# Optimization experiments

Hardware: AMD Instinct MI355X
Metric: run time of the kernel (lower is better)

The kernel has to match this reference:

```python
import jax, jax.numpy as jnp
import numpy as np

DIM = 1024
HEADS = 16
DIM_HEAD = 64
INNER = HEADS * DIM_HEAD  # 1024
SCALE = DIM_HEAD ** -0.5


def setup_inputs() -> dict:
    key = jax.random.key(0)
    ks = jax.random.split(key, 5)
    b, n = 4, 2048
    x = jax.random.normal(ks[0], (b, n, DIM), dtype=jnp.float32)
    # nn.Linear weights, stored as (in, out) for x @ W
    w_q = jax.random.normal(ks[1], (DIM, INNER), dtype=jnp.float32) / np.sqrt(DIM)
    w_kv = jax.random.normal(ks[2], (DIM, 2 * DIM_HEAD), dtype=jnp.float32) / np.sqrt(DIM)
    w_out = jax.random.normal(ks[3], (INNER, DIM), dtype=jnp.float32) / np.sqrt(INNER)
    b_out = jax.random.normal(ks[4], (DIM,), dtype=jnp.float32) * 0.01
    return {"x": x, "w_q": w_q, "w_kv": w_kv, "w_out": w_out, "b_out": b_out}


def reference(x, w_q, w_kv, w_out, b_out):
    b, n, _ = x.shape
    # Q: [b, h, n, d]; K/V: single shared head [b, n, d]
    q = (x @ w_q).reshape(b, n, HEADS, DIM_HEAD).transpose(0, 2, 1, 3)
    kv = x @ w_kv  # [b, n, 2d]
    k, v = kv[..., :DIM_HEAD], kv[..., DIM_HEAD:]
    # scores: broadcast shared K across heads
    dots = jnp.einsum('bhnd,bmd->bhnm', q, k) * SCALE  # [b,h,n,n]
    attn = jax.nn.softmax(dots, axis=-1)
    out = jnp.einsum('bhnm,bmd->bhnd', attn, v)  # shared V across heads
    out = out.transpose(0, 2, 1, 3).reshape(b, n, INNER)
    return out @ w_out + b_out
```

## Files before the change

### kernel.cpp

```cpp
#include <hip/hip_runtime.h>
#include <hip/hip_bf16.h>
#include <stdint.h>

#define SEQ    2048
#define NBATCH 4
#define NHEADS 16
#define DHEAD  64
#define MODELD 1024
#define QKVN   1152
#define MROWS  (NBATCH*SEQ)
#define SCALE_LOG2E 0.1803368801111244f

typedef __bf16 bf16x8 __attribute__((ext_vector_type(8)));
typedef float  f32x4  __attribute__((ext_vector_type(4)));

typedef __attribute__((address_space(1))) void* as1_void_p;
typedef __attribute__((address_space(3))) void* as3_void_p;

__device__ __forceinline__ void gld_lds16(const void* g, void* l) {
  __builtin_amdgcn_global_load_lds((as1_void_p)(g), (as3_void_p)(l), 16, 0, 0);
}

__device__ __forceinline__ ushort f2bf(float f) {
  union { float f; uint32_t i; } t; t.f = f;
  uint32_t r = (t.i + 0x7fffu + ((t.i >> 16) & 1u)) >> 16;
  return (ushort)r;
}
__device__ __forceinline__ uint32_t pack_bf16(float a, float b) {
  union { __hip_bfloat162 h2; uint32_t u; } cv;
  cv.h2 = __float22bfloat162_rn(make_float2(a, b));
  return cv.u;
}

__device__ __forceinline__ void do_transpose(const float* __restrict__ src,
                                             ushort* __restrict__ dst,
                                             int R, int C, float scale,
                                             int gx, int gy, int tid) {
  __shared__ float tile[32][33];
  const int tx = tid & 31, ty = tid >> 5;
  const int c0 = gx * 32, r0 = gy * 32;
#pragma unroll
  for (int j = 0; j < 4; j++)
    tile[ty*4 + j][tx] = src[(size_t)(r0 + ty*4 + j) * C + c0 + tx];
  __syncthreads();
#pragma unroll
  for (int j = 0; j < 4; j++)
    dst[(size_t)(c0 + ty*4 + j) * R + r0 + tx] = f2bf(tile[tx][ty*4 + j] * scale);
}

__global__ __launch_bounds__(256)
void prep(const float* __restrict__ x, const float* __restrict__ w_q,
          const float* __restrict__ w_kv, const float* __restrict__ w_out,
          ushort* __restrict__ xb, ushort* __restrict__ wqkvT,
          ushort* __restrict__ woutT) {
  const int bid = blockIdx.x, tid = threadIdx.x;
  if (bid < 8192) {
    const size_t i = ((size_t)bid * 256 + tid) * 4;
    const float4 v = *(const float4*)(x + i);
    ushort4 o;
    o.x = f2bf(v.x); o.y = f2bf(v.y); o.z = f2bf(v.z); o.w = f2bf(v.w);
    *(ushort4*)(xb + i) = o;
  } else if (bid < 9216) {
    const int t = bid - 8192;
    do_transpose(w_q, wqkvT, MODELD, MODELD, SCALE_LOG2E, t & 31, t >> 5, tid);
  } else if (bid < 9344) {
    const int t = bid - 9216;
    do_transpose(w_kv, wqkvT + (size_t)MODELD * MODELD, MODELD, 128, 1.0f,
                 t & 3, t >> 2, tid);
  } else {
    const int t = bid - 9344;
    do_transpose(w_out, woutT, MODELD, MODELD, 1.0f, t & 31, t >> 5, tid);
  }
}

template <bool OUT_F32>
__global__ __launch_bounds__(256)
void gemm_bt(const ushort* __restrict__ A, const ushort* __restrict__ Bt,
             void* __restrict__ Cp, const float* __restrict__ bias,
             ushort* __restrict__ VT,
             int K, int lda, int ldb, int ldc) {
  __shared__ __attribute__((aligned(16))) ushort As[128*64];
  __shared__ __attribute__((aligned(16))) ushort Bs[128*64];
  const int tid = threadIdx.x;
  const int w = tid >> 6, lane = tid & 63;
  const int quad = lane >> 4, m16 = lane & 15;

  const int nwg = gridDim.x * gridDim.y;
  const int orig = blockIdx.y * gridDim.x + blockIdx.x;
  const int qq = nwg >> 3, rr = nwg & 7;
  const int xcd = orig & 7, loc = orig >> 3;
  const int L = (xcd < rr ? xcd * (qq + 1) : rr * (qq + 1) + (xcd - rr) * qq) + loc;
  const int bm0 = (L / gridDim.x) * 128, bn0 = (L % gridDim.x) * 128;

  f32x4 acc[4][4] = {};

  const int sr = lane >> 3;
  const int sg = ((lane & 7) ^ (sr & 7)) * 8;
  const ushort* Ag = A  + (size_t)(bm0 + w*32 + sr) * lda + sg;
  const ushort* Bg = Bt + (size_t)(bn0 + w*32 + sr) * ldb + sg;
  ushort* AsW = As + (w*32)*64;
  ushort* BsW = Bs + (w*32)*64;
  const int wm = (w >> 1) * 64, wn = (w & 1) * 64;

  for (int kb = 0; kb < K; kb += 64) {
#pragma unroll
    for (int c = 0; c < 4; c++) {
      gld_lds16(Ag + (size_t)(c*8)*lda + kb, AsW + c*8*64);
      gld_lds16(Bg + (size_t)(c*8)*ldb + kb, BsW + c*8*64);
    }
    __syncthreads();
#pragma unroll
    for (int kk = 0; kk < 2; kk++) {
      bf16x8 af[4], bfr[4];
      const int rg = ((kk*4 + quad) ^ (m16 & 7)) * 8;
#pragma unroll
      for (int mi = 0; mi < 4; mi++)
        af[mi] = *(const bf16x8*)(As + (wm + mi*16 + m16)*64 + rg);
#pragma unroll
      for (int ni = 0; ni < 4; ni++)
        bfr[ni] = *(const bf16x8*)(Bs + (wn + ni*16 + m16)*64 + rg);
#pragma unroll
      for (int mi = 0; mi < 4; mi++)
#pragma unroll
        for (int ni = 0; ni < 4; ni++)
          acc[mi][ni] = __builtin_amdgcn_mfma_f32_16x16x32_bf16(
              af[mi], bfr[ni], acc[mi][ni], 0, 0, 0);
    }
    __syncthreads();
  }

  const bool blockHasV = (VT != nullptr) && (bn0 + 128 > 1088);
#pragma unroll
  for (int ni = 0; ni < 4; ni++) {
    const int col = bn0 + wn + ni*16 + m16;
    const float bv = bias ? bias[col] : 0.0f;
#pragma unroll
    for (int mi = 0; mi < 4; mi++) {
#pragma unroll
      for (int r = 0; r < 4; r++) {
        const int row = bm0 + wm + mi*16 + quad*4 + r;
        const float v = acc[mi][ni][r] + bv;
        if (OUT_F32) ((float*)Cp)[(size_t)row*ldc + col] = v;
        else         ((ushort*)Cp)[(size_t)row*ldc + col] = f2bf(v);
        if (blockHasV && col >= 1088) {
          const int d = col - 1088, bb = row >> 11, n = row & 2047;
          VT[((size_t)bb * DHEAD + d) * SEQ + n] = f2bf(v);
        }
      }
    }
  }
}

__global__ __launch_bounds__(256, 2)
void mqa_attn(const ushort* __restrict__ qkv, const ushort* __restrict__ vT,
              ushort* __restrict__ attn_out) {
  __shared__ __attribute__((aligned(16))) ushort Ks[64*72];
  __shared__ __attribute__((aligned(16))) ushort Vs[80*72];
  __shared__ __attribute__((aligned(16))) ushort pbuf[4][32*72];

  const int tid = threadIdx.x;
  const int w = tid >> 6, lane = tid & 63;
  const int quad = lane >> 4, m16 = lane & 15;
  const int h = blockIdx.y, b = blockIdx.z;
  const size_t rowbase = (size_t)b * SEQ;
  const int q0 = blockIdx.x * 128 + w * 32;
  const ushort* vTb = vT + (size_t)b * DHEAD * SEQ;
  ushort* pb = pbuf[w];

  for (int i = tid; i < 16*72; i += 256)
    Vs[64*72 + i] = (i < 72) ? (ushort)0x3F80 : (ushort)0;

  const int srow = tid >> 3, scol = (tid & 7) * 8;
  const ushort* kgbase = qkv + (rowbase + srow) * QKVN + 1024 + scol;
  const ushort* vgbase = vTb + (size_t)srow * SEQ + scol;

  bf16x8 qf[2][2];
#pragma unroll
  for (int qt = 0; qt < 2; qt++) {
    const ushort* qrow = qkv + (rowbase + q0 + qt*16 + m16) * QKVN + h * DHEAD;
    qf[qt][0] = *(const bf16x8*)(qrow + quad*8);
    qf[qt][1] = *(const bf16x8*)(qrow + 32 + quad*8);
  }

  f32x4 o[2][4] = {};
  f32x4 o4[2]   = {};

  uint4 kreg0 = *(const uint4*)(kgbase);
  uint4 kreg1 = *(const uint4*)(kgbase + (size_t)32 * QKVN);
  uint4 vreg0 = *(const uint4*)(vgbase);
  uint4 vreg1 = *(const uint4*)(vgbase + 32 * SEQ);

  for (int kv0 = 0; kv0 < SEQ; kv0 += 64) {
    __syncthreads();
    *(uint4*)(Ks + (srow     )*72 + scol) = kreg0;
    *(uint4*)(Ks + (srow + 32)*72 + scol) = kreg1;
    *(uint4*)(Vs + (srow     )*72 + scol) = vreg0;
    *(uint4*)(Vs + (srow + 32)*72 + scol) = vreg1;
    __syncthreads();

    const int kvn = (kv0 + 64) & (SEQ - 1);
    kreg0 = *(const uint4*)(kgbase + (size_t)(kvn     ) * QKVN);
    kreg1 = *(const uint4*)(kgbase + (size_t)(kvn + 32) * QKVN);
    vreg0 = *(const uint4*)(vgbase + kvn);
    vreg1 = *(const uint4*)(vgbase + 32 * SEQ + kvn);

#pragma unroll
    for (int kh = 0; kh < 2; kh++) {
#pragma unroll
      for (int t2 = 0; t2 < 2; t2++) {
        const int t = kh*2 + t2;
        const bf16x8 kf0 = *(const bf16x8*)(Ks + (t*16 + m16)*72 + quad*8);
        const bf16x8 kf1 = *(const bf16x8*)(Ks + (t*16 + m16)*72 + 32 + quad*8);
#pragma unroll
        for (int qt = 0; qt < 2; qt++) {
          f32x4 s = {};
          s = __builtin_amdgcn_mfma_f32_16x16x32_bf16(kf0, qf[qt][0], s, 0, 0, 0);
          s = __builtin_amdgcn_mfma_f32_16x16x32_bf16(kf1, qf[qt][1], s, 0, 0, 0);
          float p[4];
#pragma unroll
          for (int r = 0; r < 4; r++)
            p[r] = __builtin_amdgcn_exp2f(s[r]);
          *(uint2*)(pb + (qt*16 + m16)*72 + kh*32 + t2*16 + quad*4) =
              make_uint2(pack_bf16(p[0], p[1]), pack_bf16(p[2], p[3]));
        }
      }
    }
    asm volatile("s_waitcnt lgkmcnt(0)" ::: "memory");

#pragma unroll
    for (int kh = 0; kh < 2; kh++) {
      bf16x8 pf[2], vf[4], vf4;
#pragma unroll
      for (int qt = 0; qt < 2; qt++)
        pf[qt] = *(const bf16x8*)(pb + (qt*16 + m16)*72 + kh*32 + quad*8);
#pragma unroll
      for (int dt = 0; dt < 4; dt++)
        vf[dt] = *(const bf16x8*)(Vs + (dt*16 + m16)*72 + kh*32 + quad*8);
      vf4 = *(const bf16x8*)(Vs + (64 + m16)*72 + kh*32 + quad*8);
      __builtin_amdgcn_s_setprio(1);
#pragma unroll
      for (int qt = 0; qt < 2; qt++) {
#pragma unroll
        for (int dt = 0; dt < 4; dt++)
          o[qt][dt] = __builtin_amdgcn_mfma_f32_16x16x32_bf16(vf[dt], pf[qt], o[qt][dt], 0, 0, 0);
        o4[qt] = __builtin_amdgcn_mfma_f32_16x16x32_bf16(vf4, pf[qt], o4[qt], 0, 0, 0);
      }
      __builtin_amdgcn_s_setprio(0);
    }
  }

#pragma unroll
  for (int qt = 0; qt < 2; qt++) {
    const float l = __shfl(o4[qt][0], m16, 64);
    const float inv = 1.0f / l;
    const size_t row = rowbase + q0 + qt*16 + m16;
#pragma unroll
    for (int dt = 0; dt < 4; dt++) {
      ushort4 st;
      st.x = f2bf(o[qt][dt][0] * inv);
      st.y = f2bf(o[qt][dt][1] * inv);
      st.z = f2bf(o[qt][dt][2] * inv);
      st.w = f2bf(o[qt][dt][3] * inv);
      *(ushort4*)(attn_out + row*MODELD + h*DHEAD + dt*16 + quad*4) = st;
    }
  }
}

extern "C" void kernel_launch(void* const* d_in, const int* in_sizes, int n_in,
                              void* d_out, int out_size, void* d_ws, size_t ws_size,
                              hipStream_t stream) {
  const float* x     = (const float*)d_in[0];
  const float* w_q   = (const float*)d_in[1];
  const float* w_kv  = (const float*)d_in[2];
  const float* w_out = (const float*)d_in[3];
  const float* b_out = (const float*)d_in[4];

  ushort* wqkvT = (ushort*)d_ws;
  ushort* woutT = wqkvT + (size_t)QKVN * MODELD;
  ushort* xb    = woutT + (size_t)MODELD * MODELD;
  ushort* qkv   = xb    + (size_t)MROWS * MODELD;
  ushort* attn  = qkv   + (size_t)MROWS * QKVN;
  ushort* vTb   = attn  + (size_t)MROWS * MODELD;

  prep<<<10368, 256, 0, stream>>>(x, w_q, w_kv, w_out, xb, wqkvT, woutT);

  gemm_bt<false><<<dim3(QKVN/128, MROWS/128), 256, 0, stream>>>(
      xb, wqkvT, (void*)qkv, nullptr, vTb, MODELD, MODELD, MODELD, QKVN);

  mqa_attn<<<dim3(SEQ/128, NHEADS, NBATCH), 256, 0, stream>>>(qkv, vTb, attn);

  gemm_bt<true><<<dim3(MODELD/128, MROWS/128), 256, 0, stream>>>(
      attn, woutT, d_out, b_out, nullptr, MODELD, MODELD, MODELD, MODELD);
}
```

Before: 248.6 us.

## Load K/V MFMA fragments directly from global memory, dropping LDS staging

```diff
diff --git a/kernel.cpp b/kernel.cpp
--- a/kernel.cpp
+++ b/kernel.cpp
@@ -154,8 +154,6 @@
 __global__ __launch_bounds__(256, 2)
 void mqa_attn(const ushort* __restrict__ qkv, const ushort* __restrict__ vT,
               ushort* __restrict__ attn_out) {
-  __shared__ __attribute__((aligned(16))) ushort Ks[64*72];
-  __shared__ __attribute__((aligned(16))) ushort Vs[80*72];
   __shared__ __attribute__((aligned(16))) ushort pbuf[4][32*72];
 
   const int tid = threadIdx.x;
@@ -167,12 +165,8 @@
   const ushort* vTb = vT + (size_t)b * DHEAD * SEQ;
   ushort* pb = pbuf[w];
 
-  for (int i = tid; i < 16*72; i += 256)
-    Vs[64*72 + i] = (i < 72) ? (ushort)0x3F80 : (ushort)0;
-
-  const int srow = tid >> 3, scol = (tid & 7) * 8;
-  const ushort* kgbase = qkv + (rowbase + srow) * QKVN + 1024 + scol;
-  const ushort* vgbase = vTb + (size_t)srow * SEQ + scol;
+  const ushort* kfb = qkv + (rowbase + m16) * QKVN + 1024 + quad*8;
+  const ushort* vfb = vTb + (size_t)m16 * SEQ + quad*8;
 
   bf16x8 qf[2][2];
 #pragma unroll
@@ -182,35 +176,23 @@
     qf[qt][1] = *(const bf16x8*)(qrow + 32 + quad*8);
   }
 
+  union { ushort s[8]; bf16x8 v; } onesu;
+#pragma unroll
+  for (int j = 0; j < 8; j++) onesu.s[j] = (m16 == 0) ? (ushort)0x3F80 : (ushort)0;
+  const bf16x8 vf4c = onesu.v;
+
   f32x4 o[2][4] = {};
   f32x4 o4[2]   = {};
 
-  uint4 kreg0 = *(const uint4*)(kgbase);
-  uint4 kreg1 = *(const uint4*)(kgbase + (size_t)32 * QKVN);
-  uint4 vreg0 = *(const uint4*)(vgbase);
-  uint4 vreg1 = *(const uint4*)(vgbase + 32 * SEQ);
-
   for (int kv0 = 0; kv0 < SEQ; kv0 += 64) {
-    __syncthreads();
-    *(uint4*)(Ks + (srow     )*72 + scol) = kreg0;
-    *(uint4*)(Ks + (srow + 32)*72 + scol) = kreg1;
-    *(uint4*)(Vs + (srow     )*72 + scol) = vreg0;
-    *(uint4*)(Vs + (srow + 32)*72 + scol) = vreg1;
-    __syncthreads();
-
-    const int kvn = (kv0 + 64) & (SEQ - 1);
-    kreg0 = *(const uint4*)(kgbase + (size_t)(kvn     ) * QKVN);
-    kreg1 = *(const uint4*)(kgbase + (size_t)(kvn + 32) * QKVN);
-    vreg0 = *(const uint4*)(vgbase + kvn);
-    vreg1 = *(const uint4*)(vgbase + 32 * SEQ + kvn);
-
 #pragma unroll
     for (int kh = 0; kh < 2; kh++) {
 #pragma unroll
       for (int t2 = 0; t2 < 2; t2++) {
         const int t = kh*2 + t2;
-        const bf16x8 kf0 = *(const bf16x8*)(Ks + (t*16 + m16)*72 + quad*8);
-        const bf16x8 kf1 = *(const bf16x8*)(Ks + (t*16 + m16)*72 + 32 + quad*8);
+        const ushort* kr = kfb + (size_t)(kv0 + t*16) * QKVN;
+        const bf16x8 kf0 = *(const bf16x8*)(kr);
+        const bf16x8 kf1 = *(const bf16x8*)(kr + 32);
 #pragma unroll
         for (int qt = 0; qt < 2; qt++) {
           f32x4 s = {};
@@ -229,21 +211,20 @@
 
 #pragma unroll
     for (int kh = 0; kh < 2; kh++) {
-      bf16x8 pf[2], vf[4], vf4;
+      bf16x8 pf[2], vf[4];
 #pragma unroll
       for (int qt = 0; qt < 2; qt++)
         pf[qt] = *(const bf16x8*)(pb + (qt*16 + m16)*72 + kh*32 + quad*8);
 #pragma unroll
       for (int dt = 0; dt < 4; dt++)
-        vf[dt] = *(const bf16x8*)(Vs + (dt*16 + m16)*72 + kh*32 + quad*8);
-      vf4 = *(const bf16x8*)(Vs + (64 + m16)*72 + kh*32 + quad*8);
+        vf[dt] = *(const bf16x8*)(vfb + (size_t)(dt*16) * SEQ + kv0 + kh*32);
       __builtin_amdgcn_s_setprio(1);
 #pragma unroll
       for (int qt = 0; qt < 2; qt++) {
 #pragma unroll
         for (int dt = 0; dt < 4; dt++)
           o[qt][dt] = __builtin_amdgcn_mfma_f32_16x16x32_bf16(vf[dt], pf[qt], o[qt][dt], 0, 0, 0);
-        o4[qt] = __builtin_amdgcn_mfma_f32_16x16x32_bf16(vf4, pf[qt], o4[qt], 0, 0, 0);
+        o4[qt] = __builtin_amdgcn_mfma_f32_16x16x32_bf16(vf4c, pf[qt], o4[qt], 0, 0, 0);
       }
       __builtin_amdgcn_s_setprio(0);
     }
```

Result: slower. 388.7 us (+56.4%).
